# Optimization experiments

Hardware: AMD Instinct MI355X
Metric: run time of the kernel (lower is better)

## Reference

```python
import jax, jax.numpy as jnp
import numpy as np

WINDOW = 48
RES = 50
PRED = 96

def setup_inputs() -> dict:
    key = jax.random.key(0)
    k1, k2, k3, k4, k5 = jax.random.split(key, 5)
    x = jax.random.normal(k1, (2048, 4800, 1), dtype=jnp.float32)
    W_lin = jax.random.normal(k2, (WINDOW, WINDOW), dtype=jnp.float32) * 0.1
    # W_in = inv(P) @ B with P orthogonal, B ~ U(-1,1); statistically a dense random matrix
    W_in = jax.random.uniform(k3, (RES, WINDOW), dtype=jnp.float32, minval=-1.0, maxval=1.0)
    # diagonal reservoir weights d ~ U(-0.95, 0.95)
    d = jax.random.uniform(k4, (RES,), dtype=jnp.float32, minval=-0.95, maxval=0.95)
    W_out = jax.random.normal(k5, (PRED, RES), dtype=jnp.float32) * 0.1
    return {"x": x, "W_lin": W_lin, "W_in": W_in, "d": d, "W_out": W_out}

def reference(x, W_lin, W_in, d, W_out):
    B, S, C = x.shape  # C == 1 (non-individual path requires squeeze(1))
    seg = S // WINDOW
    # permute(0,2,1) -> view(B, C, seg, WINDOW) -> squeeze(1)
    u = x[..., 0].reshape(B, seg, WINDOW)
    # input linear (no bias): u @ W_lin.T
    u = jnp.einsum('bsw,vw->bsv', u, W_lin)
    # input projection into reservoir: W_in @ u_t for every step (one big GEMM)
    v = jnp.einsum('bsw,rw->bsr', u, W_in)  # [B, seg, RES]
    # ESN state persists across the batch loop too (never reset in update_state),
    # so the recurrence is one serial chain over B*seg steps.
    v_flat = v.reshape(B * seg, RES)
    def step(state, vt):
        # activation is LeakyReLU(negative_slope=1.0) == identity
        new = vt + d * state
        return new, new
    _, states = jax.lax.scan(step, jnp.zeros((RES,), dtype=v.dtype), v_flat)
    states = states.reshape(B, seg, RES)
    last = states[:, -1, :]              # [B, RES]
    out = last @ W_out.T                 # [B, PRED]
    return out[:, :, None]               # unsqueeze(1).permute(0,2,1) -> [B, PRED, 1]
```

## Files before the change

kernel.cpp:

```cpp
#include <hip/hip_runtime.h>

#define WINDOW 48
#define RES 50
#define PRED 96
#define BATCH 2048
#define KTOT 4800
#define KPAD 5120
#define KTRUNC 12
#define KS 10
#define KRB 480

typedef __attribute__((ext_vector_type(8))) short short8v;
typedef __attribute__((ext_vector_type(4))) float f32x4;

#define OFF_DK 0
#define OFF_WT 800
#define OFF_KB 5600
#define OFF_LP 169440
#define OFF_L  1480160

__device__ __forceinline__ float ipow(float b, int n) {
    float r = 1.f, p = b;
    while (n) { if (n & 1) r *= p; p *= p; n >>= 1; }
    return r;
}

__global__ __launch_bounds__(256) void k0(const float* __restrict__ W_lin,
                                          const float* __restrict__ W_in,
                                          const float* __restrict__ d,
                                          const float* __restrict__ W_out,
                                          float* __restrict__ ws) {
    unsigned f = blockIdx.x * 256 + threadIdx.x;
    if (f < 800) {
        int k = f / RES, r = f % RES;
        ws[OFF_DK + f] = ipow(ipow(d[r], 100), k);
    } else if (f < 5600) {
        int e = f - 800;
        int r = e / PRED, o = e % PRED;
        ws[OFF_WT + e] = W_out[o * RES + r];
    }
    if (f < 64u * KPAD) {
        int c = f / KPAD, k = f - (f / KPAD) * KPAD;
        float val = 0.f;
        if (c < RES && k < KTOT) {
            int j = k / WINDOW, w = k - j * WINDOW;
            float m = 0.f;
            for (int v = 0; v < WINDOW; ++v)
                m = fmaf(W_in[c * WINDOW + v], W_lin[v * WINDOW + w], m);
            val = ipow(d[c], 99 - j) * m;
        }
        unsigned u = __builtin_bit_cast(unsigned, val);
        ((unsigned short*)(ws + OFF_KB))[f] =
            (unsigned short)((u + 0x7FFFu + ((u >> 16) & 1u)) >> 16);
    }
}

__global__ __launch_bounds__(256, 3) void k1_mfma(const float* __restrict__ x,
                                                  const float* __restrict__ ws,
                                                  float* __restrict__ lp) {
    __shared__ float Ps[4 * 16 * 68];
    const unsigned short* Kb = (const unsigned short*)(ws + OFF_KB);
    int bid = blockIdx.x;
    int mt = bid / KS, s = bid - mt * KS;
    int b0 = mt * 16, kb = s * KRB;
    int t = threadIdx.x, w = t >> 6, l = t & 63;
    int row16 = l & 15, kq = l >> 4;
    int nst = (w == 3) ? 3 : 4;
    int kw = kb + w * 128 + kq * 8;

    const float* ap = x + (size_t)(b0 + row16) * KTOT + kw;
    const unsigned short* kp = Kb + (size_t)row16 * KPAD + kw;

    f32x4 A0[4], A1[4];
    short8v B0[4], B1[4], B2[4], B3[4];
#pragma unroll
    for (int st = 0; st < 4; ++st) if (st < nst) {
        A0[st] = *(const f32x4*)(ap + st * 32);
        A1[st] = *(const f32x4*)(ap + st * 32 + 4);
        B0[st] = *(const short8v*)(kp + (size_t)0  * KPAD + st * 32);
        B1[st] = *(const short8v*)(kp + (size_t)16 * KPAD + st * 32);
        B2[st] = *(const short8v*)(kp + (size_t)32 * KPAD + st * 32);
        B3[st] = *(const short8v*)(kp + (size_t)48 * KPAD + st * 32);
    }

    f32x4 acc0 = (f32x4)(0.f), acc1 = (f32x4)(0.f), acc2 = (f32x4)(0.f), acc3 = (f32x4)(0.f);
#pragma unroll
    for (int st = 0; st < 4; ++st) if (st < nst) {
        short8v ahi, alo;
#pragma unroll
        for (int m = 0; m < 8; ++m) {
            float v = (m < 4) ? A0[st][m] : A1[st][m - 4];
            unsigned u = __builtin_bit_cast(unsigned, v);
            unsigned hb = (u + 0x7FFFu + ((u >> 16) & 1u)) & 0xFFFF0000u;
            ahi[m] = (short)(hb >> 16);
            float r = v - __builtin_bit_cast(float, hb);
            unsigned u2 = __builtin_bit_cast(unsigned, r);
            alo[m] = (short)((u2 + 0x7FFFu + ((u2 >> 16) & 1u)) >> 16);
        }
        acc0 = __builtin_amdgcn_mfma_f32_16x16x32_bf16(ahi, B0[st], acc0, 0, 0, 0);
        acc0 = __builtin_amdgcn_mfma_f32_16x16x32_bf16(alo, B0[st], acc0, 0, 0, 0);
        acc1 = __builtin_amdgcn_mfma_f32_16x16x32_bf16(ahi, B1[st], acc1, 0, 0, 0);
        acc1 = __builtin_amdgcn_mfma_f32_16x16x32_bf16(alo, B1[st], acc1, 0, 0, 0);
        acc2 = __builtin_amdgcn_mfma_f32_16x16x32_bf16(ahi, B2[st], acc2, 0, 0, 0);
        acc2 = __builtin_amdgcn_mfma_f32_16x16x32_bf16(alo, B2[st], acc2, 0, 0, 0);
        acc3 = __builtin_amdgcn_mfma_f32_16x16x32_bf16(ahi, B3[st], acc3, 0, 0, 0);
        acc3 = __builtin_amdgcn_mfma_f32_16x16x32_bf16(alo, B3[st], acc3, 0, 0, 0);
    }

    float* P = Ps + w * 1088;
#pragma unroll
    for (int i = 0; i < 4; ++i) {
        int rr = (kq * 4 + i) * 68;
        P[rr + row16]      = acc0[i];
        P[rr + row16 + 16] = acc1[i];
        P[rr + row16 + 32] = acc2[i];
        P[rr + row16 + 48] = acc3[i];
    }
    __syncthreads();
#pragma unroll
    for (int i = 0; i < 4; ++i) {
        int o = t + i * 256;
        int r = o >> 6, c = o & 63;
        float sum = (Ps[r * 68 + c] + Ps[1088 + r * 68 + c])
                  + (Ps[2176 + r * 68 + c] + Ps[3264 + r * 68 + c]);
        lp[((size_t)s * BATCH + b0 + r) * 64 + c] = sum;
    }
}

__global__ __launch_bounds__(256) void k2a(float* __restrict__ ws) {
    int e = blockIdx.x * 256 + threadIdx.x;
    const f32x4* lp4 = (const f32x4*)(ws + OFF_LP);
    f32x4 sum = lp4[e];
#pragma unroll
    for (int sp = 1; sp < KS; ++sp)
        sum += lp4[(size_t)sp * 32768 + e];
    ((f32x4*)(ws + OFF_L))[e] = sum;
}

__global__ __launch_bounds__(128) void k2b(const float* __restrict__ ws,
                                           float* __restrict__ out) {
    const float* L  = ws + OFF_L;
    const float* Dk = ws + OFF_DK;
    const float* Wt = ws + OFF_WT;
    __shared__ float s_s[52];
    int b = blockIdx.x;
    int t = threadIdx.x;
    if (t < RES) {
        float acc = 0.f;
#pragma unroll
        for (int k = 0; k < KTRUNC; ++k) {
            int bb = b - k;
            if (bb >= 0) acc = fmaf(Dk[k * RES + t], L[(size_t)bb * 64 + t], acc);
        }
        s_s[t] = acc;
    }
    __syncthreads();
    if (t < PRED) {
        float acc = 0.f;
#pragma unroll 10
        for (int r = 0; r < RES; ++r)
            acc = fmaf(s_s[r], Wt[r * PRED + t], acc);
        out[b * PRED + t] = acc;
    }
}

extern "C" void kernel_launch(void* const* d_in, const int* in_sizes, int n_in,
                              void* d_out, int out_size, void* d_ws, size_t ws_size,
                              hipStream_t stream) {
    const float* x     = (const float*)d_in[0];
    const float* W_lin = (const float*)d_in[1];
    const float* W_in  = (const float*)d_in[2];
    const float* d     = (const float*)d_in[3];
    const float* W_out = (const float*)d_in[4];
    float* out = (float*)d_out;
    float* ws  = (float*)d_ws;
    float* lp  = ws + OFF_LP;

    k0<<<1280, 256, 0, stream>>>(W_lin, W_in, d, W_out, ws);
    k1_mfma<<<128 * KS, 256, 0, stream>>>(x, ws, lp);
    k2a<<<128, 256, 0, stream>>>(ws);
    k2b<<<BATCH, 128, 0, stream>>>(ws, out);
}
```

Baseline: 34.93 us.

## Split K finer with per-wave partials, software-pipeline loads, fuse reduction kernels

The main GEMM kernel now gives each wave its own 160-wide K slice (30 splits) and writes partials straight to global memory, so the shared-memory cross-wave reduction and its barrier go away. Loads are double-buffered so later stages' A and B fetches overlap the MFMA compute of earlier stages. The two tail kernels are merged into one that sums the 30 partials for a 16-row batch tile plus an 11-row halo, then applies the truncated decay and the output projection. Partials are stored with stride 50 instead of 64. The trade-off is three times more partial-sum traffic and redundant halo summation across blocks, in exchange for one fewer launch and more parallel work in the GEMM.

```diff
diff --git a/kernel.cpp b/kernel.cpp
--- a/kernel.cpp
+++ b/kernel.cpp
@@ -7,8 +7,8 @@
 #define KTOT 4800
 #define KPAD 5120
 #define KTRUNC 12
-#define KS 10
-#define KRB 480
+#define KS 30
+#define KRB 160
 
 typedef __attribute__((ext_vector_type(8))) short short8v;
 typedef __attribute__((ext_vector_type(4))) float f32x4;
@@ -17,7 +17,6 @@
 #define OFF_WT 800
 #define OFF_KB 5600
 #define OFF_LP 169440
-#define OFF_L  1480160
 
 __device__ __forceinline__ float ipow(float b, int n) {
     float r = 1.f, p = b;
@@ -55,112 +54,116 @@
     }
 }
 
-__global__ __launch_bounds__(256, 3) void k1_mfma(const float* __restrict__ x,
-                                                  const float* __restrict__ ws,
-                                                  float* __restrict__ lp) {
-    __shared__ float Ps[4 * 16 * 68];
+#define LOADA(st, A0, A1) { A0 = *(const f32x4*)(ap + (st) * 32); \
+                            A1 = *(const f32x4*)(ap + (st) * 32 + 4); }
+#define LOADB(st, B0, B1, B2, B3) { const unsigned short* p_ = bp + (st) * 32; \
+    B0 = *(const short8v*)p_;                    B1 = *(const short8v*)(p_ + 16 * KPAD); \
+    B2 = *(const short8v*)(p_ + 32 * KPAD);      B3 = *(const short8v*)(p_ + 48 * KPAD); }
+#define COMPUTE(A0, A1, B0, B1, B2, B3) { \
+    short8v ahi, alo; \
+    _Pragma("unroll") \
+    for (int m_ = 0; m_ < 8; ++m_) { \
+        float v_ = (m_ < 4) ? A0[m_] : A1[m_ - 4]; \
+        unsigned u_ = __builtin_bit_cast(unsigned, v_); \
+        unsigned hb_ = (u_ + 0x7FFFu + ((u_ >> 16) & 1u)) & 0xFFFF0000u; \
+        ahi[m_] = (short)(hb_ >> 16); \
+        float r_ = v_ - __builtin_bit_cast(float, hb_); \
+        unsigned u2_ = __builtin_bit_cast(unsigned, r_); \
+        alo[m_] = (short)((u2_ + 0x7FFFu + ((u2_ >> 16) & 1u)) >> 16); \
+    } \
+    acc0 = __builtin_amdgcn_mfma_f32_16x16x32_bf16(ahi, B0, acc0, 0, 0, 0); \
+    acc0 = __builtin_amdgcn_mfma_f32_16x16x32_bf16(alo, B0, acc0, 0, 0, 0); \
+    acc1 = __builtin_amdgcn_mfma_f32_16x16x32_bf16(ahi, B1, acc1, 0, 0, 0); \
+    acc1 = __builtin_amdgcn_mfma_f32_16x16x32_bf16(alo, B1, acc1, 0, 0, 0); \
+    acc2 = __builtin_amdgcn_mfma_f32_16x16x32_bf16(ahi, B2, acc2, 0, 0, 0); \
+    acc2 = __builtin_amdgcn_mfma_f32_16x16x32_bf16(alo, B2, acc2, 0, 0, 0); \
+    acc3 = __builtin_amdgcn_mfma_f32_16x16x32_bf16(ahi, B3, acc3, 0, 0, 0); \
+    acc3 = __builtin_amdgcn_mfma_f32_16x16x32_bf16(alo, B3, acc3, 0, 0, 0); }
+
+__global__ __launch_bounds__(128, 4) void k1p(const float* __restrict__ x,
+                                              const float* __restrict__ ws,
+                                              float* __restrict__ lp) {
     const unsigned short* Kb = (const unsigned short*)(ws + OFF_KB);
     int bid = blockIdx.x;
-    int mt = bid / KS, s = bid - mt * KS;
-    int b0 = mt * 16, kb = s * KRB;
-    int t = threadIdx.x, w = t >> 6, l = t & 63;
+    int mt = bid / 15, sg = bid - mt * 15;
+    int t = threadIdx.x;
+    int w = t >> 6, l = t & 63;
+    int s = sg * 2 + w;
+    int b0 = mt * 16;
     int row16 = l & 15, kq = l >> 4;
-    int nst = (w == 3) ? 3 : 4;
-    int kw = kb + w * 128 + kq * 8;
+    int kw = s * KRB + kq * 8;
 
     const float* ap = x + (size_t)(b0 + row16) * KTOT + kw;
-    const unsigned short* kp = Kb + (size_t)row16 * KPAD + kw;
-
-    f32x4 A0[4], A1[4];
-    short8v B0[4], B1[4], B2[4], B3[4];
-#pragma unroll
-    for (int st = 0; st < 4; ++st) if (st < nst) {
-        A0[st] = *(const f32x4*)(ap + st * 32);
-        A1[st] = *(const f32x4*)(ap + st * 32 + 4);
-        B0[st] = *(const short8v*)(kp + (size_t)0  * KPAD + st * 32);
-        B1[st] = *(const short8v*)(kp + (size_t)16 * KPAD + st * 32);
-        B2[st] = *(const short8v*)(kp + (size_t)32 * KPAD + st * 32);
-        B3[st] = *(const short8v*)(kp + (size_t)48 * KPAD + st * 32);
-    }
+    const unsigned short* bp = Kb + (size_t)row16 * KPAD + kw;
 
     f32x4 acc0 = (f32x4)(0.f), acc1 = (f32x4)(0.f), acc2 = (f32x4)(0.f), acc3 = (f32x4)(0.f);
-#pragma unroll
-    for (int st = 0; st < 4; ++st) if (st < nst) {
-        short8v ahi, alo;
-#pragma unroll
-        for (int m = 0; m < 8; ++m) {
-            float v = (m < 4) ? A0[st][m] : A1[st][m - 4];
-            unsigned u = __builtin_bit_cast(unsigned, v);
-            unsigned hb = (u + 0x7FFFu + ((u >> 16) & 1u)) & 0xFFFF0000u;
-            ahi[m] = (short)(hb >> 16);
-            float r = v - __builtin_bit_cast(float, hb);
-            unsigned u2 = __builtin_bit_cast(unsigned, r);
-            alo[m] = (short)((u2 + 0x7FFFu + ((u2 >> 16) & 1u)) >> 16);
-        }
-        acc0 = __builtin_amdgcn_mfma_f32_16x16x32_bf16(ahi, B0[st], acc0, 0, 0, 0);
-        acc0 = __builtin_amdgcn_mfma_f32_16x16x32_bf16(alo, B0[st], acc0, 0, 0, 0);
-        acc1 = __builtin_amdgcn_mfma_f32_16x16x32_bf16(ahi, B1[st], acc1, 0, 0, 0);
-        acc1 = __builtin_amdgcn_mfma_f32_16x16x32_bf16(alo, B1[st], acc1, 0, 0, 0);
-        acc2 = __builtin_amdgcn_mfma_f32_16x16x32_bf16(ahi, B2[st], acc2, 0, 0, 0);
-        acc2 = __builtin_amdgcn_mfma_f32_16x16x32_bf16(alo, B2[st], acc2, 0, 0, 0);
-        acc3 = __builtin_amdgcn_mfma_f32_16x16x32_bf16(ahi, B3[st], acc3, 0, 0, 0);
-        acc3 = __builtin_amdgcn_mfma_f32_16x16x32_bf16(alo, B3[st], acc3, 0, 0, 0);
-    }
 
-    float* P = Ps + w * 1088;
+    f32x4 a0s0, a1s0, a0s1, a1s1, a0s2, a1s2;
+    short8v b0s0, b1s0, b2s0, b3s0, b0s1, b1s1, b2s1, b3s1, b0s2, b1s2, b2s2, b3s2;
+
+    LOADA(0, a0s0, a1s0) LOADB(0, b0s0, b1s0, b2s0, b3s0)
+    LOADA(1, a0s1, a1s1) LOADB(1, b0s1, b1s1, b2s1, b3s1)
+    LOADA(2, a0s2, a1s2) LOADB(2, b0s2, b1s2, b2s2, b3s2)
+
+    COMPUTE(a0s0, a1s0, b0s0, b1s0, b2s0, b3s0)
+    LOADA(3, a0s0, a1s0) LOADB(3, b0s0, b1s0, b2s0, b3s0)
+    COMPUTE(a0s1, a1s1, b0s1, b1s1, b2s1, b3s1)
+    LOADA(4, a0s1, a1s1) LOADB(4, b0s1, b1s1, b2s1, b3s1)
+    COMPUTE(a0s2, a1s2, b0s2, b1s2, b2s2, b3s2)
+    COMPUTE(a0s0, a1s0, b0s0, b1s0, b2s0, b3s0)
+    COMPUTE(a0s1, a1s1, b0s1, b1s1, b2s1, b3s1)
+
+    float* dst = lp + ((size_t)s * BATCH + b0) * 50;
 #pragma unroll
     for (int i = 0; i < 4; ++i) {
-        int rr = (kq * 4 + i) * 68;
-        P[rr + row16]      = acc0[i];
-        P[rr + row16 + 16] = acc1[i];
-        P[rr + row16 + 32] = acc2[i];
-        P[rr + row16 + 48] = acc3[i];
-    }
-    __syncthreads();
-#pragma unroll
-    for (int i = 0; i < 4; ++i) {
-        int o = t + i * 256;
-        int r = o >> 6, c = o & 63;
-        float sum = (Ps[r * 68 + c] + Ps[1088 + r * 68 + c])
-                  + (Ps[2176 + r * 68 + c] + Ps[3264 + r * 68 + c]);
-        lp[((size_t)s * BATCH + b0 + r) * 64 + c] = sum;
+        int r = kq * 4 + i;
+        dst[(size_t)r * 50 + row16]      = acc0[i];
+        dst[(size_t)r * 50 + row16 + 16] = acc1[i];
+        dst[(size_t)r * 50 + row16 + 32] = acc2[i];
+        if (row16 < 2) dst[(size_t)r * 50 + row16 + 48] = acc3[i];
     }
 }
 
-__global__ __launch_bounds__(256) void k2a(float* __restrict__ ws) {
-    int e = blockIdx.x * 256 + threadIdx.x;
-    const f32x4* lp4 = (const f32x4*)(ws + OFF_LP);
-    f32x4 sum = lp4[e];
-#pragma unroll
-    for (int sp = 1; sp < KS; ++sp)
-        sum += lp4[(size_t)sp * 32768 + e];
-    ((f32x4*)(ws + OFF_L))[e] = sum;
-}
-
-__global__ __launch_bounds__(128) void k2b(const float* __restrict__ ws,
-                                           float* __restrict__ out) {
-    const float* L  = ws + OFF_L;
+__global__ __launch_bounds__(256) void k2(const float* __restrict__ ws,
+                                          float* __restrict__ out) {
+    __shared__ float Ls[27 * 52];
+    __shared__ float Ss[16 * 52];
+    const float* lp = ws + OFF_LP;
     const float* Dk = ws + OFF_DK;
     const float* Wt = ws + OFF_WT;
-    __shared__ float s_s[52];
-    int b = blockIdx.x;
+    int B0 = blockIdx.x * 16;
     int t = threadIdx.x;
-    if (t < RES) {
+
+    for (int e = t; e < 27 * 50; e += 256) {
+        int lr = e / 50, c = e - lr * 50;
+        int bb = B0 - 11 + lr;
+        float sum = 0.f;
+        if (bb >= 0) {
+#pragma unroll
+            for (int sp = 0; sp < KS; ++sp)
+                sum += lp[((size_t)sp * BATCH + bb) * 50 + c];
+        }
+        Ls[lr * 52 + c] = sum;
+    }
+    __syncthreads();
+
+    for (int e = t; e < 16 * 50; e += 256) {
+        int i = e / 50, r = e - i * 50;
         float acc = 0.f;
 #pragma unroll
-        for (int k = 0; k < KTRUNC; ++k) {
-            int bb = b - k;
-            if (bb >= 0) acc = fmaf(Dk[k * RES + t], L[(size_t)bb * 64 + t], acc);
-        }
-        s_s[t] = acc;
+        for (int k = 0; k < KTRUNC; ++k)
+            acc = fmaf(Dk[k * RES + r], Ls[(11 + i - k) * 52 + r], acc);
+        Ss[i * 52 + r] = acc;
     }
     __syncthreads();
-    if (t < PRED) {
+
+    for (int e = t; e < 16 * PRED; e += 256) {
+        int i = e / PRED, o = e - i * PRED;
         float acc = 0.f;
 #pragma unroll 10
         for (int r = 0; r < RES; ++r)
-            acc = fmaf(s_s[r], Wt[r * PRED + t], acc);
-        out[b * PRED + t] = acc;
+            acc = fmaf(Ss[i * 52 + r], Wt[r * PRED + o], acc);
+        out[(B0 + i) * PRED + o] = acc;
     }
 }
 
@@ -177,7 +180,6 @@
     float* lp  = ws + OFF_LP;
 
     k0<<<1280, 256, 0, stream>>>(W_lin, W_in, d, W_out, ws);
-    k1_mfma<<<128 * KS, 256, 0, stream>>>(x, ws, lp);
-    k2a<<<128, 256, 0, stream>>>(ws);
-    k2b<<<BATCH, 128, 0, stream>>>(ws, out);
+    k1p<<<128 * 15, 128, 0, stream>>>(x, ws, lp);
+    k2<<<128, 256, 0, stream>>>(ws, out);
 }
```

New measurement: 41.03 us. 1.17x slower.
